# Optimization experiments

Measured on AMD Instinct MI355X. Metric: run time of the kernel, lower is better.

The kernel has to match this reference:

```python
import jax, jax.numpy as jnp
import numpy as np

BATCH, DIN, HID = 32768, 64, 1024


def setup_inputs() -> dict:
    key = jax.random.key(0)
    ks = jax.random.split(key, 8)
    s_in = 1.0 / np.sqrt(DIN)
    s_h = 1.0 / np.sqrt(HID)
    return {
        "z": jax.random.normal(ks[0], (BATCH, DIN), dtype=jnp.float32),
        # Hamiltonian net: DIN -> HID -> HID -> 1
        "W1": jax.random.normal(ks[1], (DIN, HID), dtype=jnp.float32) * s_in,
        "b1": jnp.zeros((HID,), jnp.float32),
        "W2": jax.random.normal(ks[2], (HID, HID), dtype=jnp.float32) * s_h,
        "b2": jnp.zeros((HID,), jnp.float32),
        "W3": jax.random.normal(ks[3], (HID, 1), dtype=jnp.float32) * s_h,
        "b3": jnp.zeros((1,), jnp.float32),
        # Forcing net: DIN -> HID -> DIN
        "Wf1": jax.random.normal(ks[4], (DIN, HID), dtype=jnp.float32) * s_in,
        "bf1": jnp.zeros((HID,), jnp.float32),
        "Wf2": jax.random.normal(ks[5], (HID, DIN), dtype=jnp.float32) * s_h,
        "bf2": jnp.zeros((DIN,), jnp.float32),
    }


def reference(z, W1, b1, W2, b2, W3, b3, Wf1, bf1, Wf2, bf2):
    def H_sum(zz):
        h1 = jnp.tanh(zz @ W1 + b1)          # [B, HID]
        h2 = jnp.tanh(h1 @ W2 + b2)          # [B, HID]
        return jnp.sum(h2 @ W3 + b3)         # scalar (sum of H over batch)

    gradH = jax.grad(H_sum)(z)               # [B, DIN]
    dim = z.shape[1] // 2
    # symplectic combine: dq/dt = dH/dp, dp/dt = -dH/dq
    hnn_term = jnp.concatenate([gradH[:, dim:], -gradH[:, :dim]], axis=-1)
    forcing_term = jnp.tanh(z @ Wf1 + bf1) @ Wf2 + bf2  # [B, DIN]
    return hnn_term + forcing_term
```

## Files before the change

### kernel.cpp

```cpp
#include <hip/hip_runtime.h>


typedef __attribute__((ext_vector_type(8))) short s16x8;
typedef __attribute__((ext_vector_type(4))) float f32x4;
typedef unsigned short u16;

#define DEVFN static __device__ __forceinline__

constexpr int DIN = 64;
constexpr int HID = 1024;

DEVFN u16 f2bf(float f) {
  unsigned u = __builtin_bit_cast(unsigned, f);
  u += 0x7fffu + ((u >> 16) & 1u);
  return (u16)(u >> 16);
}
DEVFN float bf2f(u16 h) {
  unsigned u = ((unsigned)h) << 16;
  return __builtin_bit_cast(float, u);
}
DEVFN float fast_tanh(float x) {
  float e = __builtin_amdgcn_exp2f(x * 2.8853900817779268f);
  return 1.0f - 2.0f * __builtin_amdgcn_rcpf(e + 1.0f);
}
DEVFN f32x4 mfma16(s16x8 a, s16x8 b, f32x4 c) {
  return __builtin_amdgcn_mfma_f32_16x16x32_bf16(a, b, c, 0, 0, 0);
}

#define GLOAD16(g, l) __builtin_amdgcn_global_load_lds( \
    (const __attribute__((address_space(1))) unsigned int*)(const void*)(g), \
    (__attribute__((address_space(3))) unsigned int*)(void*)(l), 16, 0, 0)

__global__ __launch_bounds__(256) void k0_prep(
    const float* W1, const float* W2, const float* Wf1, const float* Wf2,
    u16* W1p, u16* Wf1p, u16* W2tp, u16* W2c, u16* W1c, u16* Wf2p) {
  int id = blockIdx.x * 256 + threadIdx.x;
  {
    int n = id >> 10, k = id & 1023;
    W2tp[id] = f2bf(W2[k * HID + n]);
    W2c[id]  = f2bf(W2[id]);
  }
  if (id < 65536) {
    int n = id >> 6, k = id & 63;
    W1p[id]  = f2bf(W1[k * HID + n]);
    Wf1p[id] = f2bf(Wf1[k * HID + n]);
    W1c[id]  = f2bf(W1[id]);
    int n2 = id >> 10, k2 = id & 1023;
    Wf2p[id] = f2bf(Wf2[k2 * DIN + n2]);
  }
}

__global__ __launch_bounds__(256) void k1_h1(const float* z, const u16* W1p,
                                             const float* b1, u16* h1) {
  __shared__ __align__(16) u16 zl[64 * 72];
  const int tid = threadIdx.x;
  const int lane = tid & 63, w = tid >> 6;
  const int nb = blockIdx.x & 7, mb = blockIdx.x >> 3;
  const size_t m0 = (size_t)mb * 64;
  const int n0 = nb * 128;
#pragma unroll
  for (int c = 0; c < 4; ++c) {
    int i4 = c * 256 + tid;
    int row = i4 >> 4, col4 = (i4 & 15) * 4;
    f32x4 v = *reinterpret_cast<const f32x4*>(z + (m0 + row) * DIN + col4);
    u16* d = zl + row * 72 + col4;
    d[0] = f2bf(v[0]); d[1] = f2bf(v[1]); d[2] = f2bf(v[2]); d[3] = f2bf(v[3]);
  }
  __syncthreads();
  f32x4 acc[8] = {};
#pragma unroll
  for (int kk = 0; kk < 2; ++kk) {
    const int karr = kk * 32 + ((lane >> 4) << 3);
    s16x8 a = *reinterpret_cast<const s16x8*>(zl + (16 * w + (lane & 15)) * 72 + karr);
#pragma unroll
    for (int fn = 0; fn < 8; ++fn) {
      int n = n0 + fn * 16 + (lane & 15);
      s16x8 b = *reinterpret_cast<const s16x8*>(W1p + (size_t)n * 64 + karr);
      acc[fn] = mfma16(a, b, acc[fn]);
    }
  }
#pragma unroll
  for (int fn = 0; fn < 8; ++fn) {
    int n = n0 + fn * 16 + (lane & 15);
    float bias = b1[n];
#pragma unroll
    for (int j = 0; j < 4; ++j) {
      size_t m = m0 + 16 * w + ((lane >> 4) << 2) + j;
      h1[m * HID + n] = f2bf(fast_tanh(acc[fn][j] + bias));
    }
  }
}

template <int MODE>
__global__ __launch_bounds__(512, 2) void k23_gemm(
    const u16* __restrict__ A, const u16* __restrict__ Bp,
    const float* __restrict__ b2, const float* __restrict__ W3,
    const u16* __restrict__ h1in, u16* __restrict__ outb) {
  extern __shared__ u16 lds[];
  const int tid = threadIdx.x;
  const int lane = tid & 63, w = tid >> 6;
  const int wr = w >> 2, wc = w & 3;
  const int xcd = blockIdx.x & 7, local = blockIdx.x >> 3;
  const size_t m0 = (size_t)(xcd * 16 + (local >> 2)) * 256;
  const int n0 = (local & 3) * 256;

  const u16* gpa[4]; const u16* gpb[4]; int lo[4];
#pragma unroll
  for (int c = 0; c < 4; ++c) {
    int idx = c * 512 + tid, row = idx >> 3, cg = idx & 7;
    int sc = (cg ^ (row & 7)) << 3;
    gpa[c] = A + (m0 + row) * 1024 + sc;
    gpb[c] = Bp + (size_t)(n0 + row) * 1024 + sc;
    lo[c] = idx * 8;
  }
#define STAGE_A(B_, T_) { _Pragma("unroll") for (int c = 0; c < 4; ++c) \
    GLOAD16(gpa[c] + (T_) * 64, lds + (B_) * 32768 + lo[c]); }
#define STAGE_B(B_, T_) { _Pragma("unroll") for (int c = 0; c < 4; ++c) \
    GLOAD16(gpb[c] + (T_) * 64, lds + (B_) * 32768 + 16384 + lo[c]); }

  const int swz = (lane & 7) << 3;
  int aoff[8], boff[4];
#pragma unroll
  for (int i = 0; i < 8; ++i)
    aoff[i] = (wr * 128 + i * 16 + (lane & 15)) * 64 + ((lane >> 4) << 3);
#pragma unroll
  for (int j = 0; j < 4; ++j)
    boff[j] = (wc * 64 + j * 16 + (lane & 15)) * 64 + ((lane >> 4) << 3);

  f32x4 acc[8][4] = {};

#define PHASE(B_, KK_) { \
    s16x8 af[8], bf[4]; \
    _Pragma("unroll") for (int i = 0; i < 8; ++i) \
      af[i] = *reinterpret_cast<const s16x8*>(lds + (B_) * 32768 + ((aoff[i] + (KK_) * 32) ^ swz)); \
    _Pragma("unroll") for (int j = 0; j < 4; ++j) \
      bf[j] = *reinterpret_cast<const s16x8*>(lds + (B_) * 32768 + 16384 + ((boff[j] + (KK_) * 32) ^ swz)); \
    __builtin_amdgcn_s_setprio(1); \
    _Pragma("unroll") for (int i = 0; i < 8; ++i) { \
      _Pragma("unroll") for (int j = 0; j < 4; ++j) \
        acc[i][j] = mfma16(af[i], bf[j], acc[i][j]); } \
    __builtin_amdgcn_s_setprio(0); }

  STAGE_A(0, 0); STAGE_B(0, 0);
  for (int t = 0; t < 15; ++t) {
    const int cur = t & 1, nxt = cur ^ 1;
    STAGE_A(nxt, t + 1);
    asm volatile("s_waitcnt vmcnt(4)" ::: "memory");
    __builtin_amdgcn_s_barrier();
    asm volatile("" ::: "memory");
    PHASE(cur, 0);
    STAGE_B(nxt, t + 1);
    PHASE(cur, 1);
    asm volatile("" ::: "memory");
    __builtin_amdgcn_s_barrier();
    asm volatile("" ::: "memory");
  }
  asm volatile("s_waitcnt vmcnt(0)" ::: "memory");
  __builtin_amdgcn_s_barrier();
  asm volatile("" ::: "memory");
  PHASE(1, 0);
  PHASE(1, 1);
  asm volatile("" ::: "memory");
  __builtin_amdgcn_s_barrier();
  asm volatile("" ::: "memory");

  const int wbase = w * 8192;
  float b2v[4], w3v[4];
  if (MODE == 0) {
#pragma unroll
    for (int j = 0; j < 4; ++j) {
      int n = n0 + wc * 64 + j * 16 + (lane & 15);
      b2v[j] = b2[n]; w3v[j] = W3[n];
    }
  }
#pragma unroll
  for (int h = 0; h < 2; ++h) {
    if (h == 1) asm volatile("s_waitcnt lgkmcnt(0)" ::: "memory");
#pragma unroll
    for (int ip = 0; ip < 4; ++ip) {
#pragma unroll
      for (int j = 0; j < 4; ++j) {
#pragma unroll
        for (int r = 0; r < 4; ++r) {
          float v = acc[h * 4 + ip][j][r];
          u16 o;
          if (MODE == 0) {
            float tt = fast_tanh(v + b2v[j]);
            o = f2bf(w3v[j] * (1.f - tt * tt));
          } else {
            o = f2bf(v);
          }
          int lr = ip * 16 + ((lane >> 4) << 2) + r;
          lds[wbase + lr * 64 + j * 16 + (lane & 15)] = o;
        }
      }
    }
#pragma unroll
    for (int r8 = 0; r8 < 8; ++r8) {
      int lr = r8 * 8 + (lane >> 3), c8 = (lane & 7) * 8;
      s16x8 vv = *reinterpret_cast<const s16x8*>(lds + wbase + lr * 64 + c8);
      size_t grow = m0 + wr * 128 + h * 64 + lr;
      int gcol = n0 + wc * 64 + c8;
      if (MODE == 1) {
        s16x8 hh = *reinterpret_cast<const s16x8*>(h1in + grow * 1024 + gcol);
#pragma unroll
        for (int e = 0; e < 8; ++e) {
          float hv = bf2f((u16)hh[e]);
          vv[e] = (short)f2bf(bf2f((u16)vv[e]) * (1.f - hv * hv));
        }
      }
      *reinterpret_cast<s16x8*>(outb + grow * 1024 + gcol) = vv;
    }
  }
#undef STAGE_A
#undef STAGE_B
#undef PHASE
}

__global__ __launch_bounds__(256) void k4_final(
    const float* z, const u16* gp1, const u16* Wf1p, const u16* Wf2p,
    const u16* W1c, const float* bf1, const float* bf2, float* out) {
  __shared__ __align__(16) u16 zl[64 * 72];
  __shared__ __align__(16) u16 f1l[64 * 72];
  __shared__ __align__(16) u16 gl[64 * 64];
  const int tid = threadIdx.x;
  const int lane = tid & 63, w = tid >> 6;
  const size_t m0 = (size_t)blockIdx.x * 64;
#pragma unroll
  for (int c = 0; c < 4; ++c) {
    int i4 = c * 256 + tid;
    int row = i4 >> 4, col4 = (i4 & 15) * 4;
    f32x4 v = *reinterpret_cast<const f32x4*>(z + (m0 + row) * DIN + col4);
    u16* d = zl + row * 72 + col4;
    d[0] = f2bf(v[0]); d[1] = f2bf(v[1]); d[2] = f2bf(v[2]); d[3] = f2bf(v[3]);
  }
  __syncthreads();
  f32x4 facc[4] = {};
  f32x4 hacc[4] = {};
  for (int kc = 0; kc < 16; ++kc) {
    const int kbase = kc * 64;
    f32x4 pacc[4] = {};
#pragma unroll
    for (int kk = 0; kk < 2; ++kk) {
      const int karr = kk * 32 + ((lane >> 4) << 3);
      s16x8 a = *reinterpret_cast<const s16x8*>(zl + (16 * w + (lane & 15)) * 72 + karr);
#pragma unroll
      for (int fn = 0; fn < 4; ++fn) {
        int n = kbase + fn * 16 + (lane & 15);
        s16x8 b = *reinterpret_cast<const s16x8*>(Wf1p + (size_t)n * 64 + karr);
        pacc[fn] = mfma16(a, b, pacc[fn]);
      }
    }
#pragma unroll
    for (int fn = 0; fn < 4; ++fn) {
      int nloc = fn * 16 + (lane & 15);
      float bias = bf1[kbase + nloc];
#pragma unroll
      for (int j = 0; j < 4; ++j) {
        int r = 16 * w + ((lane >> 4) << 2) + j;
        f1l[r * 72 + nloc] = f2bf(fast_tanh(pacc[fn][j] + bias));
      }
    }
    __syncthreads();
#pragma unroll
    for (int c = 0; c < 2; ++c) {
      int idx = c * 256 + tid;
      int row = idx >> 3, k8 = (idx & 7) << 3;
      GLOAD16(gp1 + (m0 + row) * 1024 + kbase + k8, gl + idx * 8);
    }
#pragma unroll
    for (int kk = 0; kk < 2; ++kk) {
      const int karr = kk * 32 + ((lane >> 4) << 3);
      s16x8 af = *reinterpret_cast<const s16x8*>(f1l + (16 * w + (lane & 15)) * 72 + karr);
#pragma unroll
      for (int fn = 0; fn < 4; ++fn) {
        int n = fn * 16 + (lane & 15);
        s16x8 b = *reinterpret_cast<const s16x8*>(Wf2p + (size_t)n * 1024 + kbase + karr);
        facc[fn] = mfma16(af, b, facc[fn]);
      }
    }
    __syncthreads();
#pragma unroll
    for (int kk = 0; kk < 2; ++kk) {
      const int karr = kk * 32 + ((lane >> 4) << 3);
      s16x8 ag = *reinterpret_cast<const s16x8*>(gl + (16 * w + (lane & 15)) * 64 + karr);
#pragma unroll
      for (int fn = 0; fn < 4; ++fn) {
        int n = fn * 16 + (lane & 15);
        s16x8 b = *reinterpret_cast<const s16x8*>(W1c + (size_t)n * 1024 + kbase + karr);
        hacc[fn] = mfma16(ag, b, hacc[fn]);
      }
    }
  }
#pragma unroll
  for (int fn = 0; fn < 4; ++fn) {
    int n = fn * 16 + (lane & 15);
    float bias = bf2[n];
    float sgn = (fn < 2) ? 1.f : -1.f;
#pragma unroll
    for (int j = 0; j < 4; ++j) {
      size_t m = m0 + 16 * w + ((lane >> 4) << 2) + j;
      out[m * DIN + n] = facc[fn][j] + bias + sgn * hacc[(fn + 2) & 3][j];
    }
  }
}

extern "C" void kernel_launch(void* const* d_in, const int* in_sizes, int n_in,
                              void* d_out, int out_size, void* d_ws, size_t ws_size,
                              hipStream_t stream) {
  const float* z   = (const float*)d_in[0];
  const float* W1  = (const float*)d_in[1];
  const float* b1  = (const float*)d_in[2];
  const float* W2  = (const float*)d_in[3];
  const float* b2  = (const float*)d_in[4];
  const float* W3  = (const float*)d_in[5];
  const float* Wf1 = (const float*)d_in[7];
  const float* bf1 = (const float*)d_in[8];
  const float* Wf2 = (const float*)d_in[9];
  const float* bf2 = (const float*)d_in[10];

  char* ws = (char*)d_ws;
  u16* W1p  = (u16*)(ws + 0);
  u16* Wf1p = (u16*)(ws + 131072);
  u16* W2tp = (u16*)(ws + 262144);
  u16* W2c  = (u16*)(ws + 2359296);
  u16* W1c  = (u16*)(ws + 4456448);
  u16* Wf2p = (u16*)(ws + 4587520);
  u16* h1   = (u16*)(ws + 4718592);
  u16* gp2  = (u16*)(ws + 4718592 + 67108864);
  float* out = (float*)d_out;

  k0_prep<<<4096, 256, 0, stream>>>(W1, W2, Wf1, Wf2, W1p, Wf1p, W2tp, W2c, W1c, Wf2p);
  k1_h1<<<4096, 256, 0, stream>>>(z, W1p, b1, h1);
  k23_gemm<0><<<512, 512, 131072, stream>>>(h1, W2tp, b2, W3, nullptr, gp2);
  k23_gemm<1><<<512, 512, 131072, stream>>>(gp2, W2c, nullptr, nullptr, h1, h1);
  k4_final<<<512, 256, 0, stream>>>(z, h1, Wf1p, Wf2p, W1c, bf1, bf2, out);
}
```

Baseline: 306.0 us.

## Split k4 reduction across wave pairs and drop block-wide LDS staging

The final kernel now gives each wave its own 16 rows and half of the hidden dimension. Two waves split the K range and combine their partial accumulators through shared memory once at the end, and the grid doubles to 1024 blocks. z and gp1 fragments are loaded straight from global memory into registers instead of being staged in LDS. The per-wave tanh tile uses an XOR-swizzled layout, so the per-iteration __syncthreads are gone. The aim is more parallelism and fewer barriers, at the cost of a final LDS reduction and uncoalesced direct global fragment loads.

```diff
diff --git a/kernel.cpp b/kernel.cpp
--- a/kernel.cpp
+++ b/kernel.cpp
@@ -218,89 +218,110 @@
 }
 
 __global__ __launch_bounds__(256) void k4_final(
-    const float* z, const u16* gp1, const u16* Wf1p, const u16* Wf2p,
-    const u16* W1c, const float* bf1, const float* bf2, float* out) {
-  __shared__ __align__(16) u16 zl[64 * 72];
-  __shared__ __align__(16) u16 f1l[64 * 72];
-  __shared__ __align__(16) u16 gl[64 * 64];
+    const float* __restrict__ z, const u16* __restrict__ gp1,
+    const u16* __restrict__ Wf1p, const u16* __restrict__ Wf2p,
+    const u16* __restrict__ W1c, const float* __restrict__ bf1,
+    const float* __restrict__ bf2, float* __restrict__ out) {
+  __shared__ u16 f1l[4][1024];
+  __shared__ float red[2][64][33];
   const int tid = threadIdx.x;
   const int lane = tid & 63, w = tid >> 6;
-  const size_t m0 = (size_t)blockIdx.x * 64;
-#pragma unroll
-  for (int c = 0; c < 4; ++c) {
-    int i4 = c * 256 + tid;
-    int row = i4 >> 4, col4 = (i4 & 15) * 4;
-    f32x4 v = *reinterpret_cast<const f32x4*>(z + (m0 + row) * DIN + col4);
-    u16* d = zl + row * 72 + col4;
-    d[0] = f2bf(v[0]); d[1] = f2bf(v[1]); d[2] = f2bf(v[2]); d[3] = f2bf(v[3]);
-  }
-  __syncthreads();
+  const int wpair = w >> 1, half = w & 1;
+  const int lr = lane & 15, g = lane >> 4;
+  const size_t m0 = (size_t)blockIdx.x * 32 + wpair * 16;
+  u16* fl = f1l[w];
+
+  s16x8 za[2];
+#pragma unroll
+  for (int kk = 0; kk < 2; ++kk) {
+    const float* src = z + (m0 + lr) * DIN + kk * 32 + g * 8;
+    f32x4 v0 = *reinterpret_cast<const f32x4*>(src);
+    f32x4 v1 = *reinterpret_cast<const f32x4*>(src + 4);
+    s16x8 t;
+    t[0] = (short)f2bf(v0[0]); t[1] = (short)f2bf(v0[1]);
+    t[2] = (short)f2bf(v0[2]); t[3] = (short)f2bf(v0[3]);
+    t[4] = (short)f2bf(v1[0]); t[5] = (short)f2bf(v1[1]);
+    t[6] = (short)f2bf(v1[2]); t[7] = (short)f2bf(v1[3]);
+    za[kk] = t;
+  }
+
   f32x4 facc[4] = {};
   f32x4 hacc[4] = {};
-  for (int kc = 0; kc < 16; ++kc) {
+  const int kc_lo = half * 8, kc_hi = kc_lo + 8;
+#pragma unroll 2
+  for (int kc = kc_lo; kc < kc_hi; ++kc) {
     const int kbase = kc * 64;
     f32x4 pacc[4] = {};
 #pragma unroll
     for (int kk = 0; kk < 2; ++kk) {
-      const int karr = kk * 32 + ((lane >> 4) << 3);
-      s16x8 a = *reinterpret_cast<const s16x8*>(zl + (16 * w + (lane & 15)) * 72 + karr);
 #pragma unroll
       for (int fn = 0; fn < 4; ++fn) {
-        int n = kbase + fn * 16 + (lane & 15);
-        s16x8 b = *reinterpret_cast<const s16x8*>(Wf1p + (size_t)n * 64 + karr);
-        pacc[fn] = mfma16(a, b, pacc[fn]);
+        int n = kbase + fn * 16 + lr;
+        s16x8 b = *reinterpret_cast<const s16x8*>(Wf1p + (size_t)n * 64 + kk * 32 + g * 8);
+        pacc[fn] = mfma16(za[kk], b, pacc[fn]);
       }
     }
 #pragma unroll
     for (int fn = 0; fn < 4; ++fn) {
-      int nloc = fn * 16 + (lane & 15);
-      float bias = bf1[kbase + nloc];
-#pragma unroll
-      for (int j = 0; j < 4; ++j) {
-        int r = 16 * w + ((lane >> 4) << 2) + j;
-        f1l[r * 72 + nloc] = f2bf(fast_tanh(pacc[fn][j] + bias));
-      }
-    }
-    __syncthreads();
-#pragma unroll
-    for (int c = 0; c < 2; ++c) {
-      int idx = c * 256 + tid;
-      int row = idx >> 3, k8 = (idx & 7) << 3;
-      GLOAD16(gp1 + (m0 + row) * 1024 + kbase + k8, gl + idx * 8);
-    }
+      float bias = bf1[kbase + fn * 16 + lr];
+#pragma unroll
+      for (int j = 0; j < 4; ++j) {
+        int r = g * 4 + j;
+        int c = fn * 16 + lr;
+        fl[r * 64 + (c ^ ((r & 7) << 3))] = f2bf(fast_tanh(pacc[fn][j] + bias));
+      }
+    }
+    asm volatile("s_waitcnt lgkmcnt(0)" ::: "memory");
+    __builtin_amdgcn_sched_barrier(0);
 #pragma unroll
     for (int kk = 0; kk < 2; ++kk) {
-      const int karr = kk * 32 + ((lane >> 4) << 3);
-      s16x8 af = *reinterpret_cast<const s16x8*>(f1l + (16 * w + (lane & 15)) * 72 + karr);
+      int c0 = (kk * 32 + g * 8) ^ ((lr & 7) << 3);
+      s16x8 a = *reinterpret_cast<const s16x8*>(fl + lr * 64 + c0);
 #pragma unroll
       for (int fn = 0; fn < 4; ++fn) {
-        int n = fn * 16 + (lane & 15);
-        s16x8 b = *reinterpret_cast<const s16x8*>(Wf2p + (size_t)n * 1024 + kbase + karr);
-        facc[fn] = mfma16(af, b, facc[fn]);
-      }
-    }
-    __syncthreads();
+        s16x8 b = *reinterpret_cast<const s16x8*>(Wf2p + (size_t)(fn * 16 + lr) * 1024 + kbase + kk * 32 + g * 8);
+        facc[fn] = mfma16(a, b, facc[fn]);
+      }
+    }
 #pragma unroll
     for (int kk = 0; kk < 2; ++kk) {
-      const int karr = kk * 32 + ((lane >> 4) << 3);
-      s16x8 ag = *reinterpret_cast<const s16x8*>(gl + (16 * w + (lane & 15)) * 64 + karr);
+      s16x8 ag = *reinterpret_cast<const s16x8*>(gp1 + (m0 + lr) * 1024 + kbase + kk * 32 + g * 8);
 #pragma unroll
       for (int fn = 0; fn < 4; ++fn) {
-        int n = fn * 16 + (lane & 15);
-        s16x8 b = *reinterpret_cast<const s16x8*>(W1c + (size_t)n * 1024 + kbase + karr);
+        s16x8 b = *reinterpret_cast<const s16x8*>(W1c + (size_t)(fn * 16 + lr) * 1024 + kbase + kk * 32 + g * 8);
         hacc[fn] = mfma16(ag, b, hacc[fn]);
       }
     }
   }
-#pragma unroll
-  for (int fn = 0; fn < 4; ++fn) {
-    int n = fn * 16 + (lane & 15);
-    float bias = bf2[n];
-    float sgn = (fn < 2) ? 1.f : -1.f;
-#pragma unroll
-    for (int j = 0; j < 4; ++j) {
-      size_t m = m0 + 16 * w + ((lane >> 4) << 2) + j;
-      out[m * DIN + n] = facc[fn][j] + bias + sgn * hacc[(fn + 2) & 3][j];
+
+  if (half == 1) {
+#pragma unroll
+    for (int fn = 0; fn < 4; ++fn)
+#pragma unroll
+      for (int j = 0; j < 4; ++j) {
+        red[wpair][lane][fn * 4 + j] = facc[fn][j];
+        red[wpair][lane][16 + fn * 4 + j] = hacc[fn][j];
+      }
+  }
+  __syncthreads();
+  if (half == 0) {
+#pragma unroll
+    for (int fn = 0; fn < 4; ++fn)
+#pragma unroll
+      for (int j = 0; j < 4; ++j) {
+        facc[fn][j] += red[wpair][lane][fn * 4 + j];
+        hacc[fn][j] += red[wpair][lane][16 + fn * 4 + j];
+      }
+#pragma unroll
+    for (int fn = 0; fn < 4; ++fn) {
+      int n = fn * 16 + lr;
+      float bias = bf2[n];
+      float sgn = (fn < 2) ? 1.f : -1.f;
+#pragma unroll
+      for (int j = 0; j < 4; ++j) {
+        size_t m = m0 + g * 4 + j;
+        out[m * DIN + n] = facc[fn][j] + bias + sgn * hacc[(fn + 2) & 3][j];
+      }
     }
   }
 }
@@ -334,5 +355,5 @@
   k1_h1<<<4096, 256, 0, stream>>>(z, W1p, b1, h1);
   k23_gemm<0><<<512, 512, 131072, stream>>>(h1, W2tp, b2, W3, nullptr, gp2);
   k23_gemm<1><<<512, 512, 131072, stream>>>(gp2, W2c, nullptr, nullptr, h1, h1);
-  k4_final<<<512, 256, 0, stream>>>(z, h1, Wf1p, Wf2p, W1c, bf1, bf2, out);
-}
+  k4_final<<<1024, 256, 0, stream>>>(z, h1, Wf1p, Wf2p, W1c, bf1, bf2, out);
+}
```

Result: faster. 287.1 us (-6.2%).

## Fold symplectic swap into W1 and split forcing net into separate GEMM

Applied to the files above, without the earlier changes.

The symplectic permutation and sign flip are folded into a pre-signed, row-swapped copy of W1. This lets the gradient term and the forcing term share one accumulator in a concatenated K=2048 GEMM. The forcing hidden layer tanh(z@Wf1+bf1) is now computed by reusing the k1_h1 kernel into the gp2 buffer, instead of being recomputed inside the final kernel. The final kernel becomes a double-buffered, LDS-swizzled global_load_lds GEMM. The cost is an extra write and read of a 64 MB intermediate, traded against the serialized per-chunk tanh and three barriers per step in the old fused kernel.

```diff
diff --git a/kernel.cpp b/kernel.cpp
--- a/kernel.cpp
+++ b/kernel.cpp
@@ -33,7 +33,7 @@
 
 __global__ __launch_bounds__(256) void k0_prep(
     const float* W1, const float* W2, const float* Wf1, const float* Wf2,
-    u16* W1p, u16* Wf1p, u16* W2tp, u16* W2c, u16* W1c, u16* Wf2p) {
+    u16* W1p, u16* Wf1p, u16* W2tp, u16* W2c, u16* W1s, u16* Wf2p) {
   int id = blockIdx.x * 256 + threadIdx.x;
   {
     int n = id >> 10, k = id & 1023;
@@ -44,14 +44,15 @@
     int n = id >> 6, k = id & 63;
     W1p[id]  = f2bf(W1[k * HID + n]);
     Wf1p[id] = f2bf(Wf1[k * HID + n]);
-    W1c[id]  = f2bf(W1[id]);
-    int n2 = id >> 10, k2 = id & 1023;
-    Wf2p[id] = f2bf(Wf2[k2 * DIN + n2]);
-  }
-}
-
-__global__ __launch_bounds__(256) void k1_h1(const float* z, const u16* W1p,
-                                             const float* b1, u16* h1) {
+    int nn = id >> 10, kk2 = id & 1023;
+    float s = (nn < 32) ? 1.f : -1.f;
+    W1s[id]  = f2bf(s * W1[((nn + 32) & 63) * HID + kk2]);
+    Wf2p[id] = f2bf(Wf2[kk2 * DIN + nn]);
+  }
+}
+
+__global__ __launch_bounds__(256) void k1_h1(const float* z, const u16* Wp,
+                                             const float* b, u16* o) {
   __shared__ __align__(16) u16 zl[64 * 72];
   const int tid = threadIdx.x;
   const int lane = tid & 63, w = tid >> 6;
@@ -75,18 +76,18 @@
 #pragma unroll
     for (int fn = 0; fn < 8; ++fn) {
       int n = n0 + fn * 16 + (lane & 15);
-      s16x8 b = *reinterpret_cast<const s16x8*>(W1p + (size_t)n * 64 + karr);
-      acc[fn] = mfma16(a, b, acc[fn]);
+      s16x8 bb = *reinterpret_cast<const s16x8*>(Wp + (size_t)n * 64 + karr);
+      acc[fn] = mfma16(a, bb, acc[fn]);
     }
   }
 #pragma unroll
   for (int fn = 0; fn < 8; ++fn) {
     int n = n0 + fn * 16 + (lane & 15);
-    float bias = b1[n];
+    float bias = b[n];
 #pragma unroll
     for (int j = 0; j < 4; ++j) {
       size_t m = m0 + 16 * w + ((lane >> 4) << 2) + j;
-      h1[m * HID + n] = f2bf(fast_tanh(acc[fn][j] + bias));
+      o[m * HID + n] = f2bf(fast_tanh(acc[fn][j] + bias));
     }
   }
 }
@@ -217,92 +218,90 @@
 #undef PHASE
 }
 
-__global__ __launch_bounds__(256) void k4_final(
-    const float* z, const u16* gp1, const u16* Wf1p, const u16* Wf2p,
-    const u16* W1c, const float* bf1, const float* bf2, float* out) {
-  __shared__ __align__(16) u16 zl[64 * 72];
-  __shared__ __align__(16) u16 f1l[64 * 72];
-  __shared__ __align__(16) u16 gl[64 * 64];
+__global__ __launch_bounds__(256) void k4_gemm(
+    const u16* __restrict__ gp1, const u16* __restrict__ f1,
+    const u16* __restrict__ W1s, const u16* __restrict__ Wf2p,
+    const float* __restrict__ bf2, float* __restrict__ out) {
+  __shared__ __align__(16) u16 Ab[2][4096];
+  __shared__ __align__(16) u16 Bb[2][4096];
   const int tid = threadIdx.x;
   const int lane = tid & 63, w = tid >> 6;
+  const int lr = lane & 15, g = lane >> 4;
   const size_t m0 = (size_t)blockIdx.x * 64;
-#pragma unroll
-  for (int c = 0; c < 4; ++c) {
-    int i4 = c * 256 + tid;
-    int row = i4 >> 4, col4 = (i4 & 15) * 4;
-    f32x4 v = *reinterpret_cast<const f32x4*>(z + (m0 + row) * DIN + col4);
-    u16* d = zl + row * 72 + col4;
-    d[0] = f2bf(v[0]); d[1] = f2bf(v[1]); d[2] = f2bf(v[2]); d[3] = f2bf(v[3]);
-  }
-  __syncthreads();
-  f32x4 facc[4] = {};
-  f32x4 hacc[4] = {};
-  for (int kc = 0; kc < 16; ++kc) {
-    const int kbase = kc * 64;
-    f32x4 pacc[4] = {};
-#pragma unroll
-    for (int kk = 0; kk < 2; ++kk) {
-      const int karr = kk * 32 + ((lane >> 4) << 3);
-      s16x8 a = *reinterpret_cast<const s16x8*>(zl + (16 * w + (lane & 15)) * 72 + karr);
+
+  int aoffs[2], boffs[2], lo[2];
+#pragma unroll
+  for (int c = 0; c < 2; ++c) {
+    int idx = c * 256 + tid;
+    int row = idx >> 3, cg = idx & 7;
+    aoffs[c] = (int)((m0 + row) * 1024) + ((cg ^ (row & 7)) << 3);
+    boffs[c] = row * 1024 + ((cg ^ (row & 7)) << 3);
+    lo[c] = idx * 8;
+  }
+#define K4STAGE(B_, T_) { \
+    const u16* ab_ = (T_) < 16 ? gp1 : f1; \
+    const u16* bb_ = (T_) < 16 ? W1s : Wf2p; \
+    const int ko_ = ((T_) & 15) * 64; \
+    _Pragma("unroll") for (int c = 0; c < 2; ++c) { \
+      GLOAD16(ab_ + aoffs[c] + ko_, Ab[B_] + lo[c]); \
+      GLOAD16(bb_ + boffs[c] + ko_, Bb[B_] + lo[c]); } }
+
+  const int arow = w * 16 + lr;
+  int afr[2], bfr[2][4];
+#pragma unroll
+  for (int kkl = 0; kkl < 2; ++kkl) {
+    afr[kkl] = arow * 64 + ((kkl * 32 + g * 8) ^ ((arow & 7) << 3));
+#pragma unroll
+    for (int fn = 0; fn < 4; ++fn) {
+      int br = fn * 16 + lr;
+      bfr[kkl][fn] = br * 64 + ((kkl * 32 + g * 8) ^ ((br & 7) << 3));
+    }
+  }
+
+  f32x4 acc[4] = {};
+  K4STAGE(0, 0);
+  for (int t = 0; t < 31; ++t) {
+    const int cur = t & 1, nxt = cur ^ 1;
+    K4STAGE(nxt, t + 1);
+    asm volatile("s_waitcnt vmcnt(4)" ::: "memory");
+    __builtin_amdgcn_s_barrier();
+    asm volatile("" ::: "memory");
+#pragma unroll
+    for (int kkl = 0; kkl < 2; ++kkl) {
+      s16x8 a = *reinterpret_cast<const s16x8*>(Ab[cur] + afr[kkl]);
 #pragma unroll
       for (int fn = 0; fn < 4; ++fn) {
-        int n = kbase + fn * 16 + (lane & 15);
-        s16x8 b = *reinterpret_cast<const s16x8*>(Wf1p + (size_t)n * 64 + karr);
-        pacc[fn] = mfma16(a, b, pacc[fn]);
+        s16x8 b = *reinterpret_cast<const s16x8*>(Bb[cur] + bfr[kkl][fn]);
+        acc[fn] = mfma16(a, b, acc[fn]);
       }
     }
+    asm volatile("" ::: "memory");
+    __builtin_amdgcn_s_barrier();
+    asm volatile("" ::: "memory");
+  }
+  asm volatile("s_waitcnt vmcnt(0)" ::: "memory");
+  __builtin_amdgcn_s_barrier();
+  asm volatile("" ::: "memory");
+#pragma unroll
+  for (int kkl = 0; kkl < 2; ++kkl) {
+    s16x8 a = *reinterpret_cast<const s16x8*>(Ab[1] + afr[kkl]);
 #pragma unroll
     for (int fn = 0; fn < 4; ++fn) {
-      int nloc = fn * 16 + (lane & 15);
-      float bias = bf1[kbase + nloc];
-#pragma unroll
-      for (int j = 0; j < 4; ++j) {
-        int r = 16 * w + ((lane >> 4) << 2) + j;
-        f1l[r * 72 + nloc] = f2bf(fast_tanh(pacc[fn][j] + bias));
-      }
-    }
-    __syncthreads();
-#pragma unroll
-    for (int c = 0; c < 2; ++c) {
-      int idx = c * 256 + tid;
-      int row = idx >> 3, k8 = (idx & 7) << 3;
-      GLOAD16(gp1 + (m0 + row) * 1024 + kbase + k8, gl + idx * 8);
-    }
-#pragma unroll
-    for (int kk = 0; kk < 2; ++kk) {
-      const int karr = kk * 32 + ((lane >> 4) << 3);
-      s16x8 af = *reinterpret_cast<const s16x8*>(f1l + (16 * w + (lane & 15)) * 72 + karr);
-#pragma unroll
-      for (int fn = 0; fn < 4; ++fn) {
-        int n = fn * 16 + (lane & 15);
-        s16x8 b = *reinterpret_cast<const s16x8*>(Wf2p + (size_t)n * 1024 + kbase + karr);
-        facc[fn] = mfma16(af, b, facc[fn]);
-      }
-    }
-    __syncthreads();
-#pragma unroll
-    for (int kk = 0; kk < 2; ++kk) {
-      const int karr = kk * 32 + ((lane >> 4) << 3);
-      s16x8 ag = *reinterpret_cast<const s16x8*>(gl + (16 * w + (lane & 15)) * 64 + karr);
-#pragma unroll
-      for (int fn = 0; fn < 4; ++fn) {
-        int n = fn * 16 + (lane & 15);
-        s16x8 b = *reinterpret_cast<const s16x8*>(W1c + (size_t)n * 1024 + kbase + karr);
-        hacc[fn] = mfma16(ag, b, hacc[fn]);
-      }
+      s16x8 b = *reinterpret_cast<const s16x8*>(Bb[1] + bfr[kkl][fn]);
+      acc[fn] = mfma16(a, b, acc[fn]);
     }
   }
 #pragma unroll
   for (int fn = 0; fn < 4; ++fn) {
-    int n = fn * 16 + (lane & 15);
+    int n = fn * 16 + lr;
     float bias = bf2[n];
-    float sgn = (fn < 2) ? 1.f : -1.f;
 #pragma unroll
     for (int j = 0; j < 4; ++j) {
-      size_t m = m0 + 16 * w + ((lane >> 4) << 2) + j;
-      out[m * DIN + n] = facc[fn][j] + bias + sgn * hacc[(fn + 2) & 3][j];
-    }
-  }
+      size_t m = m0 + w * 16 + g * 4 + j;
+      out[m * DIN + n] = acc[fn][j] + bias;
+    }
+  }
+#undef K4STAGE
 }
 
 extern "C" void kernel_launch(void* const* d_in, const int* in_sizes, int n_in,
@@ -324,15 +323,16 @@
   u16* Wf1p = (u16*)(ws + 131072);
   u16* W2tp = (u16*)(ws + 262144);
   u16* W2c  = (u16*)(ws + 2359296);
-  u16* W1c  = (u16*)(ws + 4456448);
+  u16* W1s  = (u16*)(ws + 4456448);
   u16* Wf2p = (u16*)(ws + 4587520);
   u16* h1   = (u16*)(ws + 4718592);
   u16* gp2  = (u16*)(ws + 4718592 + 67108864);
   float* out = (float*)d_out;
 
-  k0_prep<<<4096, 256, 0, stream>>>(W1, W2, Wf1, Wf2, W1p, Wf1p, W2tp, W2c, W1c, Wf2p);
+  k0_prep<<<4096, 256, 0, stream>>>(W1, W2, Wf1, Wf2, W1p, Wf1p, W2tp, W2c, W1s, Wf2p);
   k1_h1<<<4096, 256, 0, stream>>>(z, W1p, b1, h1);
   k23_gemm<0><<<512, 512, 131072, stream>>>(h1, W2tp, b2, W3, nullptr, gp2);
   k23_gemm<1><<<512, 512, 131072, stream>>>(gp2, W2c, nullptr, nullptr, h1, h1);
-  k4_final<<<512, 256, 0, stream>>>(z, h1, Wf1p, Wf2p, W1c, bf1, bf2, out);
-}
+  k1_h1<<<4096, 256, 0, stream>>>(z, Wf1p, bf1, gp2);
+  k4_gemm<<<512, 256, 0, stream>>>(h1, gp2, W1s, Wf2p, bf2, out);
+}
```

After: 254.2 us. -16.9%, faster.
